# Kernel optimization log

Hardware: AMD Instinct MI355X
Metric: run time of the kernel (lower is better)

Reference implementation:

```python
import jax, jax.numpy as jnp
import numpy as np

HIDDEN = 2048
N_HEADS = 16
N_KV = 4
HEAD_DIM = 128
EPS = 1e-6
B = 8
L = 1024
PREFIX = 256
SUFFIX = L - PREFIX
N_COMPACT = PREFIX + B * SUFFIX  # 6400
T_FULL = B * L                   # 8192
ROPE_THETA = 10000.0


def _radix_indices():
    # full position (b, p) -> compact index
    scatter = np.empty(T_FULL, dtype=np.int64)
    for b in range(B):
        scatter[b * L: b * L + PREFIX] = np.arange(PREFIX)
        scatter[b * L + PREFIX: (b + 1) * L] = PREFIX + b * SUFFIX + np.arange(SUFFIX)
    # compact index -> first full occurrence
    fold = np.empty(N_COMPACT, dtype=np.int64)
    fold[:PREFIX] = np.arange(PREFIX)
    for b in range(B):
        fold[PREFIX + b * SUFFIX: PREFIX + (b + 1) * SUFFIX] = b * L + PREFIX + np.arange(SUFFIX)
    return scatter, fold


def setup_inputs() -> dict:
    key = jax.random.key(0)
    ks = jax.random.split(key, 8)
    scatter_np, fold_np = _radix_indices()
    # per-compact-token positions for RoPE
    pos = np.empty(N_COMPACT, dtype=np.float32)
    pos[:PREFIX] = np.arange(PREFIX)
    for b in range(B):
        pos[PREFIX + b * SUFFIX: PREFIX + (b + 1) * SUFFIX] = PREFIX + np.arange(SUFFIX)
    inv_freq = ROPE_THETA ** (-np.arange(HEAD_DIM // 2, dtype=np.float32) / (HEAD_DIM // 2))
    freqs = pos[:, None] * inv_freq[None, :]  # [N_c, 64]
    s = 0.02
    return {
        "hidden_states": jax.random.normal(ks[0], (N_COMPACT, HIDDEN), jnp.float32),
        "cos": jnp.asarray(np.cos(freqs), jnp.float32),
        "sin": jnp.asarray(np.sin(freqs), jnp.float32),
        "cu_seq_lengths": jnp.arange(B + 1, dtype=jnp.int32) * L,
        "max_seq_len": L,
        "fold_gather": jnp.asarray(fold_np),
        "scatter_indices": jnp.asarray(scatter_np),
        "wq": jax.random.normal(ks[1], (HIDDEN, N_HEADS * HEAD_DIM), jnp.float32) * s,
        "wk": jax.random.normal(ks[2], (HIDDEN, N_KV * HEAD_DIM), jnp.float32) * s,
        "wv": jax.random.normal(ks[3], (HIDDEN, N_KV * HEAD_DIM), jnp.float32) * s,
        "wo": jax.random.normal(ks[4], (N_HEADS * HEAD_DIM, HIDDEN), jnp.float32) * s,
        "q_norm_w": jnp.ones((HEAD_DIM,), jnp.float32),
        "k_norm_w": jnp.ones((HEAD_DIM,), jnp.float32),
    }


def _rmsnorm(x, w):
    xf = x.astype(jnp.float32)
    var = jnp.mean(xf * xf, axis=-1, keepdims=True)
    return (w * (xf * jax.lax.rsqrt(var + EPS))).astype(x.dtype)


def _rope(x, cos, sin):
    # x: [N, H, D]; cos/sin: [N, D/2]
    half = cos.shape[-1]
    x1, x2 = x[..., :half], x[..., half:2 * half]
    c, s = cos[:, None, :], sin[:, None, :]
    return jnp.concatenate([x1 * c - x2 * s, x1 * s + x2 * c], axis=-1)


def reference(hidden_states, cos, sin, cu_seq_lengths, max_seq_len,
              fold_gather, scatter_indices, wq, wk, wv, wo, q_norm_w, k_norm_w):
    N = hidden_states.shape[0]
    q = (hidden_states @ wq).reshape(N, N_HEADS, HEAD_DIM)
    k = (hidden_states @ wk).reshape(N, N_KV, HEAD_DIM)
    v = (hidden_states @ wv).reshape(N, N_KV, HEAD_DIM)
    q = _rope(_rmsnorm(q, q_norm_w), cos, sin)
    k = _rope(_rmsnorm(k, k_norm_w), cos, sin)
    # radix scatter: expand compact tokens to full varlen token stream
    qf = q[scatter_indices].reshape(B, L, N_HEADS, HEAD_DIM)
    kf = k[scatter_indices].reshape(B, L, N_KV, HEAD_DIM)
    vf = v[scatter_indices].reshape(B, L, N_KV, HEAD_DIM)
    group = N_HEADS // N_KV
    kf = jnp.repeat(kf, group, axis=2)
    vf = jnp.repeat(vf, group, axis=2)
    scale = HEAD_DIM ** -0.5
    scores = jnp.einsum('bqhd,bkhd->bhqk', qf, kf) * scale
    causal = jnp.tril(jnp.ones((L, L), dtype=bool))
    scores = jnp.where(causal[None, None], scores, jnp.finfo(scores.dtype).min)
    probs = jax.nn.softmax(scores, axis=-1)
    out = jnp.einsum('bhqk,bkhd->bqhd', probs, vf).reshape(T_FULL, N_HEADS * HEAD_DIM)
    # radix fold: gather back to compact tokens
    out_compact = out[fold_gather]
    return out_compact @ wo
```

## Files before the change

kernel.cpp:

```cpp
#include <hip/hip_runtime.h>
#include <hip/hip_bf16.h>

typedef __bf16 bf16;
typedef __bf16 bf16x4 __attribute__((ext_vector_type(4)));
typedef __bf16 bf16x8 __attribute__((ext_vector_type(8)));
typedef float f32x4 __attribute__((ext_vector_type(4)));

#define HID 2048
#define NHEADS 16
#define NKV 4
#define HD 128
#define NC 6400
#define KVW (NKV * HD)

__device__ __forceinline__ void async_cp16(const bf16* src, bf16* dst_lds) {
  __builtin_amdgcn_global_load_lds(
      (const __attribute__((address_space(1))) void*)src,
      (__attribute__((address_space(3))) void*)dst_lds, 16, 0, 0);
}

__device__ __forceinline__ void xcd_swizzle(int& bx, int& by) {
  int nx = gridDim.x;
  int nwg = nx * gridDim.y;
  int id = by * nx + bx;
  int q = nwg >> 3, r = nwg & 7;
  int xcd = id & 7, idx = id >> 3;
  int nid = (xcd < r ? xcd * (q + 1) : r * (q + 1) + (xcd - r) * q) + idx;
  bx = nid % nx;
  by = nid / nx;
}

__global__ __launch_bounds__(256) void k_cvt(const float* __restrict__ in,
                                             bf16* __restrict__ out) {
  size_t i = ((size_t)blockIdx.x * 256 + threadIdx.x) * 8;
  f32x4 a = *(const f32x4*)(in + i);
  f32x4 b = *(const f32x4*)(in + i + 4);
  bf16x8 t;
  for (int j = 0; j < 4; j++) {
    t[j] = (bf16)a[j];
    t[j + 4] = (bf16)b[j];
  }
  *(bf16x8*)(out + i) = t;
}

__global__ __launch_bounds__(256) void k_transpose(const float* __restrict__ in,
                                                   bf16* __restrict__ out,
                                                   int R, int C) {
  __shared__ bf16 tile[32][33];
  int bc = blockIdx.x * 32, br = blockIdx.y * 32;
  int tx = threadIdx.x & 31, ty = threadIdx.x >> 5;
  for (int i = 0; i < 32; i += 8)
    tile[ty + i][tx] = (bf16)in[(size_t)(br + ty + i) * C + bc + tx];
  __syncthreads();
  for (int i = 0; i < 32; i += 8)
    out[(size_t)(bc + ty + i) * R + br + tx] = tile[tx][ty + i];
}

__device__ __forceinline__ void gemm256_core(
    const bf16* __restrict__ A, const bf16* __restrict__ Bt, int m0, int nloc,
    int K, bf16* AsB, bf16* BsB, f32x4 (&acc)[2][4][4]) {
  const int tid = threadIdx.x;
  const int lane = tid & 63, wave = tid >> 6;
  const int l15 = lane & 15, quad = lane >> 4;
  const int wr = wave >> 2, wc = wave & 3;
  const int r0A = wr * 128 + l15;
  const int r0B = wc * 64 + l15;
  const int colOff0 = (quad * 8) ^ ((l15 & 7) << 3);
  const int colOff1 = (32 + quad * 8) ^ ((l15 & 7) << 3);
  const size_t offS0 =
      (size_t)(tid >> 3) * K + ((((tid & 7) ^ ((tid >> 3) & 7)) << 4) >> 1);
  const size_t offS1 = offS0 + (size_t)64 * K;
  const int dstW0 = wave * 512;
  const int dstW1 = 4096 + wave * 512;
  const bf16* Abase = A + (size_t)m0 * K;
  const bf16* Bbase = Bt + (size_t)nloc * K;
  const int KM = K - 1;

#define STAGE(gb, lds, dbuf, h, kc)                             \
  do {                                                          \
    const bf16* _s = (gb) + (size_t)(h) * 128 * K + (kc);       \
    bf16* _d = (lds) + (dbuf) * 16384 + (h) * 8192;             \
    async_cp16(_s + offS0, _d + dstW0);                         \
    async_cp16(_s + offS1, _d + dstW1);                         \
  } while (0)

#define LDA(dbuf, mh)                                           \
  do {                                                          \
    _Pragma("unroll") for (int i = 0; i < 4; i++) {             \
      int r = r0A + (mh) * 64 + i * 16;                         \
      const bf16* p = AsB + (dbuf) * 16384 + r * 64;            \
      a[i][0] = *(const bf16x8*)(p + colOff0);                  \
      a[i][1] = *(const bf16x8*)(p + colOff1);                  \
    }                                                           \
  } while (0)

#define LDB(dbuf, nh, bb)                                       \
  do {                                                          \
    _Pragma("unroll") for (int j = 0; j < 2; j++) {             \
      int r = r0B + (nh) * 32 + j * 16;                         \
      const bf16* p = BsB + (dbuf) * 16384 + r * 64;            \
      bb[j][0] = *(const bf16x8*)(p + colOff0);                 \
      bb[j][1] = *(const bf16x8*)(p + colOff1);                 \
    }                                                           \
  } while (0)

#define MFMAQ(mh, nh, bb)                                                    \
  do {                                                                       \
    __builtin_amdgcn_s_setprio(1);                                           \
    _Pragma("unroll") for (int i = 0; i < 4; i++)                            \
        _Pragma("unroll") for (int j = 0; j < 2; j++) {                      \
      acc[mh][i][(nh) * 2 + j] = __builtin_amdgcn_mfma_f32_16x16x32_bf16(    \
          a[i][0], bb[j][0], acc[mh][i][(nh) * 2 + j], 0, 0, 0);             \
      acc[mh][i][(nh) * 2 + j] = __builtin_amdgcn_mfma_f32_16x16x32_bf16(    \
          a[i][1], bb[j][1], acc[mh][i][(nh) * 2 + j], 0, 0, 0);             \
    }                                                                        \
    __builtin_amdgcn_s_setprio(0);                                           \
  } while (0)

  STAGE(Abase, AsB, 0, 0, 0);
  STAGE(Abase, AsB, 0, 1, 0);
  STAGE(Bbase, BsB, 0, 0, 0);
  STAGE(Bbase, BsB, 0, 1, 0);
  STAGE(Bbase, BsB, 1, 0, 64);
  STAGE(Bbase, BsB, 1, 1, 64);
  STAGE(Abase, AsB, 1, 0, 64);
  asm volatile("s_waitcnt vmcnt(6)" ::: "memory");
  __builtin_amdgcn_s_barrier();

  bf16x8 a[4][2], b0[2][2], b1[2][2];

  const int NIT = K >> 7;
#pragma unroll 1
  for (int it = 0; it < NIT; ++it) {
    const int kb = it << 7;
    LDA(0, 0);
    LDB(0, 0, b0);
    STAGE(Abase, AsB, 1, 1, (kb + 64) & KM);
    asm volatile("s_waitcnt lgkmcnt(8)");
    __builtin_amdgcn_s_barrier();
    asm volatile("s_waitcnt lgkmcnt(0)" ::: "memory");
    MFMAQ(0, 0, b0);
    __builtin_amdgcn_s_barrier();
    LDB(0, 1, b1);
    __builtin_amdgcn_s_barrier();
    asm volatile("s_waitcnt lgkmcnt(0)" ::: "memory");
    MFMAQ(0, 1, b1);
    __builtin_amdgcn_s_barrier();
    LDA(0, 1);
    STAGE(Bbase, BsB, 0, 0, (kb + 128) & KM);
    __builtin_amdgcn_s_barrier();
    asm volatile("s_waitcnt lgkmcnt(0)" ::: "memory");
    MFMAQ(1, 0, b0);
    __builtin_amdgcn_s_barrier();
    STAGE(Bbase, BsB, 0, 1, (kb + 128) & KM);
    __builtin_amdgcn_s_barrier();
    asm volatile("s_waitcnt lgkmcnt(0)" ::: "memory");
    MFMAQ(1, 1, b1);
    asm volatile("s_waitcnt vmcnt(4)" ::: "memory");
    __builtin_amdgcn_s_barrier();
    LDA(1, 0);
    LDB(1, 0, b0);
    STAGE(Abase, AsB, 0, 0, (kb + 128) & KM);
    asm volatile("s_waitcnt lgkmcnt(8)");
    __builtin_amdgcn_s_barrier();
    asm volatile("s_waitcnt lgkmcnt(0)" ::: "memory");
    MFMAQ(0, 0, b0);
    __builtin_amdgcn_s_barrier();
    LDB(1, 1, b1);
    STAGE(Abase, AsB, 0, 1, (kb + 128) & KM);
    __builtin_amdgcn_s_barrier();
    asm volatile("s_waitcnt lgkmcnt(0)" ::: "memory");
    MFMAQ(0, 1, b1);
    __builtin_amdgcn_s_barrier();
    LDA(1, 1);
    STAGE(Bbase, BsB, 1, 0, (kb + 192) & KM);
    __builtin_amdgcn_s_barrier();
    asm volatile("s_waitcnt lgkmcnt(0)" ::: "memory");
    MFMAQ(1, 0, b0);
    __builtin_amdgcn_s_barrier();
    STAGE(Bbase, BsB, 1, 1, (kb + 192) & KM);
    STAGE(Abase, AsB, 1, 0, (kb + 192) & KM);
    __builtin_amdgcn_s_barrier();
    asm volatile("s_waitcnt lgkmcnt(0)" ::: "memory");
    MFMAQ(1, 1, b1);
    asm volatile("s_waitcnt vmcnt(6)" ::: "memory");
    __builtin_amdgcn_s_barrier();
  }
#undef STAGE
#undef LDA
#undef LDB
#undef MFMAQ
}

__global__ __launch_bounds__(512, 2) void k_proj(const bf16* __restrict__ A,
                                                 const bf16* __restrict__ wqT,
                                                 const bf16* __restrict__ wkT,
                                                 const bf16* __restrict__ wvT,
                                                 bf16* __restrict__ qb,
                                                 bf16* __restrict__ kb,
                                                 bf16* __restrict__ vtb) {
  __shared__ __align__(16) bf16 smem[2][2][256][64];
  int bx = blockIdx.x, by = blockIdx.y;
  xcd_swizzle(bx, by);
  int n0 = bx * 256, m0 = by * 256;

  const bf16* bt;
  int nloc, outsel;
  if (n0 < HID) {
    bt = wqT; nloc = n0; outsel = 0;
  } else if (n0 < HID + KVW) {
    bt = wkT; nloc = n0 - HID; outsel = 1;
  } else {
    bt = wvT; nloc = n0 - HID - KVW; outsel = 2;
  }

  const f32x4 fz = {0.0f, 0.0f, 0.0f, 0.0f};
  f32x4 acc[2][4][4];
#pragma unroll
  for (int mh = 0; mh < 2; mh++)
#pragma unroll
    for (int i = 0; i < 4; i++)
#pragma unroll
      for (int j = 0; j < 4; j++) acc[mh][i][j] = fz;

  gemm256_core(A, bt, m0, nloc, HID, &smem[0][0][0][0], &smem[1][0][0][0], acc);

  int tid = threadIdx.x, lane = tid & 63, wave = tid >> 6;
  int l15 = lane & 15, quad = lane >> 4;
  int wr = wave >> 2, wc = wave & 3;

  if (outsel == 2) {
    asm volatile("s_waitcnt vmcnt(0)" ::: "memory");
    __syncthreads();
    bf16* sm = &smem[0][0][0][0];
#pragma unroll
    for (int mh = 0; mh < 2; mh++)
#pragma unroll
      for (int i = 0; i < 4; i++)
#pragma unroll
        for (int nj = 0; nj < 4; nj++) {
          int col = wc * 64 + nj * 16 + l15;
          int row = wr * 128 + mh * 64 + i * 16 + quad * 4;
          int idx = col * 256 + ((row + ((col & 7) << 3)) & 255);
          bf16x4 v4 = {(bf16)acc[mh][i][nj][0], (bf16)acc[mh][i][nj][1],
                       (bf16)acc[mh][i][nj][2], (bf16)acc[mh][i][nj][3]};
          *(bf16x4*)&sm[idx] = v4;
        }
    __syncthreads();
#pragma unroll
    for (int p = 0; p < 4; p++) {
      int cc = p * 64 + (tid >> 3);
      int h = tid & 7;
#pragma unroll
      for (int j = 0; j < 4; j++) {
        int row8 = h * 32 + j * 8;
        bf16x8 v =
            *(const bf16x8*)&sm[cc * 256 + ((row8 + ((cc & 7) << 3)) & 255)];
        *(bf16x8*)(vtb + (size_t)(nloc + cc) * NC + m0 + row8) = v;
      }
    }
  } else {
#pragma unroll
    for (int mh = 0; mh < 2; mh++)
#pragma unroll
      for (int i = 0; i < 4; i++)
#pragma unroll
        for (int nj = 0; nj < 4; nj++)
#pragma unroll
          for (int r = 0; r < 4; r++) {
            int row = m0 + wr * 128 + mh * 64 + i * 16 + quad * 4 + r;
            int col = nloc + wc * 64 + nj * 16 + l15;
            float v = acc[mh][i][nj][r];
            if (outsel == 0)
              qb[(size_t)row * HID + col] = (bf16)v;
            else
              kb[(size_t)row * KVW + col] = (bf16)v;
          }
  }
}

__global__ __launch_bounds__(512, 2) void k_gemm_out(const bf16* __restrict__ A,
                                                     const bf16* __restrict__ Bt,
                                                     float* __restrict__ C,
                                                     int M, int N, int K) {
  __shared__ __align__(16) bf16 smem[2][2][256][64];
  int bx = blockIdx.x, by = blockIdx.y;
  xcd_swizzle(bx, by);
  int n0 = bx * 256, m0 = by * 256;

  const f32x4 fz = {0.0f, 0.0f, 0.0f, 0.0f};
  f32x4 acc[2][4][4];
#pragma unroll
  for (int mh = 0; mh < 2; mh++)
#pragma unroll
    for (int i = 0; i < 4; i++)
#pragma unroll
      for (int j = 0; j < 4; j++) acc[mh][i][j] = fz;

  gemm256_core(A, Bt, m0, n0, K, &smem[0][0][0][0], &smem[1][0][0][0], acc);

  int tid = threadIdx.x, lane = tid & 63, wave = tid >> 6;
  int l15 = lane & 15, quad = lane >> 4;
  int wr = wave >> 2, wc = wave & 3;
#pragma unroll
  for (int mh = 0; mh < 2; mh++)
#pragma unroll
    for (int i = 0; i < 4; i++)
#pragma unroll
      for (int nj = 0; nj < 4; nj++)
#pragma unroll
        for (int r = 0; r < 4; r++) {
          int row = m0 + wr * 128 + mh * 64 + i * 16 + quad * 4 + r;
          int col = n0 + wc * 64 + nj * 16 + l15;
          C[(size_t)row * N + col] = acc[mh][i][nj][r];
        }
}

__global__ __launch_bounds__(256) void k_normrope(bf16* __restrict__ q,
                                                  bf16* __restrict__ k,
                                                  const float* __restrict__ cs,
                                                  const float* __restrict__ sn,
                                                  const float* __restrict__ qw,
                                                  const float* __restrict__ kw) {
  int pair = blockIdx.x * 4 + (threadIdx.x >> 6);
  int lane = threadIdx.x & 63;
  int n = pair / 20, hh = pair % 20;
  bf16* base;
  const float* w;
  if (hh < 16) {
    base = q + (size_t)n * HID + hh * HD;
    w = qw;
  } else {
    base = k + (size_t)n * KVW + (hh - 16) * HD;
    w = kw;
  }
  float x1 = (float)base[lane], x2 = (float)base[lane + 64];
  float ss = x1 * x1 + x2 * x2;
  for (int o = 32; o; o >>= 1) ss += __shfl_xor(ss, o);
  float inv = rsqrtf(ss * (1.0f / 128.0f) + 1e-6f);
  float x1n = x1 * inv * w[lane];
  float x2n = x2 * inv * w[lane + 64];
  float c = cs[(size_t)n * 64 + lane];
  float s = sn[(size_t)n * 64 + lane];
  base[lane] = (bf16)(x1n * c - x2n * s);
  base[lane + 64] = (bf16)(x1n * s + x2n * c);
}

__global__ __launch_bounds__(256) void k_attn(const bf16* __restrict__ qb,
                                              const bf16* __restrict__ kb,
                                              const bf16* __restrict__ vt,
                                              bf16* __restrict__ ob) {
  int t = blockIdx.x;
  int h = blockIdx.y;
  int kh = h >> 2;
  int tid = threadIdx.x;
  int lane = tid & 63, wave = tid >> 6;
  int l15 = lane & 15, quad = lane >> 4;

  int b, p0, nbase;
  if (t < 96) {
    int ti = 11 - (t >> 3);
    b = t & 7;
    p0 = 256 + ti * 64;
    nbase = 256 + b * 768 + ti * 64;
  } else {
    int pt = 99 - t;
    b = 0;
    p0 = pt * 64;
    nbase = pt * 64;
  }

  __shared__ __align__(16) bf16 Ks[2][64][128];
  __shared__ __align__(16) bf16 Vs[2][128][64];
  __shared__ __align__(16) bf16 Ps[4][16][76];

#define STAGE_KV(buf, kbase)                                                  \
  do {                                                                        \
    _Pragma("unroll") for (int i = 0; i < 4; i++) {                           \
      int rowK = wave * 16 + i * 4 + quad;                                    \
      async_cp16(kb + (size_t)((kbase) + rowK) * KVW + kh * HD +              \
                     ((l15 ^ ((i * 4 + quad) & 7)) << 3),                     \
                 &Ks[buf][0][0] + (wave * 4 + i) * 512);                      \
    }                                                                         \
    _Pragma("unroll") for (int i = 0; i < 4; i++) {                           \
      int dV = wave * 32 + i * 8 + (lane >> 3);                               \
      async_cp16(vt + (size_t)(kh * HD + dV) * NC + (kbase) +                 \
                     (((lane & 7) ^ (lane >> 3)) << 3),                       \
                 &Vs[buf][0][0] + (wave * 4 + i) * 512);                      \
    }                                                                         \
  } while (0)

  const float qscale = 0.08838834764831845f * 1.4426950408889634f;
  bf16x8 aq[4];
  {
    const bf16* qp =
        qb + (size_t)(nbase + wave * 16 + l15) * HID + h * HD + quad * 8;
#pragma unroll
    for (int ks = 0; ks < 4; ks++) {
      bf16x8 v = *(const bf16x8*)(qp + ks * 32);
#pragma unroll
      for (int e = 0; e < 8; e++) v[e] = (bf16)((float)v[e] * qscale);
      aq[ks] = v;
    }
  }
  int qpos[4];
#pragma unroll
  for (int r = 0; r < 4; r++) qpos[r] = p0 + wave * 16 + quad * 4 + r;

  const f32x4 fz = {0.0f, 0.0f, 0.0f, 0.0f};
  f32x4 oacc[8];
#pragma unroll
  for (int i = 0; i < 8; i++) oacc[i] = fz;
  float mrow[4], lrow[4];
#pragma unroll
  for (int r = 0; r < 4; r++) {
    mrow[r] = -3.0e38f;
    lrow[r] = 0.0f;
  }
  const int swzc = (l15 & 7) << 3;

  int nkt = p0 / 64 + 1;

  STAGE_KV(0, 0);
  asm volatile("s_waitcnt vmcnt(0)" ::: "memory");
  __syncthreads();

  int cur = 0;
  for (int kt = 0; kt < nkt; kt++) {
    int kpos0 = kt * 64;
    bool hasnext = (kt + 1 < nkt);
    if (hasnext) {
      int kposN = kpos0 + 64;
      int kbaseN = (kposN < 256) ? kposN : 256 + b * 768 + (kposN - 256);
      STAGE_KV(cur ^ 1, kbaseN);
      __builtin_amdgcn_sched_barrier(0);
    }

    bool diag = (kt == nkt - 1);
    float sv[4][4];
#pragma unroll
    for (int nt = 0; nt < 4; nt++) {
      f32x4 z = fz;
      __builtin_amdgcn_s_setprio(1);
#pragma unroll
      for (int ks = 0; ks < 4; ks++) {
        bf16x8 kf =
            *(const bf16x8*)&Ks[cur][nt * 16 + l15][(ks * 32 + quad * 8) ^ swzc];
        z = __builtin_amdgcn_mfma_f32_16x16x32_bf16(aq[ks], kf, z, 0, 0, 0);
      }
      __builtin_amdgcn_s_setprio(0);
#pragma unroll
      for (int r = 0; r < 4; r++) sv[nt][r] = z[r];
    }
    if (diag) {
#pragma unroll
      for (int nt = 0; nt < 4; nt++) {
        int kpos = kpos0 + nt * 16 + l15;
#pragma unroll
        for (int r = 0; r < 4; r++)
          if (kpos > qpos[r]) sv[nt][r] = -1.0e30f;
      }
    }
    float mx[4];
#pragma unroll
    for (int r = 0; r < 4; r++) {
      float m = fmaxf(fmaxf(sv[0][r], sv[1][r]), fmaxf(sv[2][r], sv[3][r]));
#pragma unroll
      for (int o = 1; o < 16; o <<= 1) m = fmaxf(m, __shfl_xor(m, o));
      mx[r] = m;
    }
    bool ok = (mx[0] <= mrow[0] + 8.0f) && (mx[1] <= mrow[1] + 8.0f) &&
              (mx[2] <= mrow[2] + 8.0f) && (mx[3] <= mrow[3] + 8.0f);
    if (!__all(ok)) {
#pragma unroll
      for (int r = 0; r < 4; r++) {
        float mnew = fmaxf(mrow[r], mx[r]);
        float alpha = exp2f(mrow[r] - mnew);
        mrow[r] = mnew;
        lrow[r] *= alpha;
#pragma unroll
        for (int i = 0; i < 8; i++) oacc[i][r] *= alpha;
      }
    }
#pragma unroll
    for (int r = 0; r < 4; r++) {
      float ps = 0.0f;
#pragma unroll
      for (int nt = 0; nt < 4; nt++) {
        float p = exp2f(sv[nt][r] - mrow[r]);
        sv[nt][r] = p;
        ps += p;
      }
#pragma unroll
      for (int o = 1; o < 16; o <<= 1) ps += __shfl_xor(ps, o);
      lrow[r] += ps;
    }

#pragma unroll
    for (int nt = 0; nt < 4; nt++)
#pragma unroll
      for (int r = 0; r < 4; r++)
        Ps[wave][quad * 4 + r][nt * 16 + l15] = (bf16)sv[nt][r];
    asm volatile("s_waitcnt lgkmcnt(0)" ::: "memory");
    bf16x8 pa[2];
#pragma unroll
    for (int ks = 0; ks < 2; ks++)
      pa[ks] = *(const bf16x8*)&Ps[wave][l15][ks * 32 + quad * 8];
    __builtin_amdgcn_s_setprio(1);
#pragma unroll
    for (int dt = 0; dt < 8; dt++)
#pragma unroll
      for (int ks = 0; ks < 2; ks++) {
        bf16x8 vf =
            *(const bf16x8*)&Vs[cur][dt * 16 + l15][(ks * 32 + quad * 8) ^ swzc];
        oacc[dt] =
            __builtin_amdgcn_mfma_f32_16x16x32_bf16(pa[ks], vf, oacc[dt], 0, 0, 0);
      }
    __builtin_amdgcn_s_setprio(0);

    if (hasnext) {
      asm volatile("s_waitcnt vmcnt(0)" ::: "memory");
      __syncthreads();
      cur ^= 1;
    }
  }
#undef STAGE_KV
#pragma unroll
  for (int r = 0; r < 4; r++) {
    float il = 1.0f / lrow[r];
    bf16* op = ob + (size_t)(nbase + wave * 16 + quad * 4 + r) * HID + h * HD;
#pragma unroll
    for (int dt = 0; dt < 8; dt++) op[dt * 16 + l15] = (bf16)(oacc[dt][r] * il);
  }
}

extern "C" void kernel_launch(void* const* d_in, const int* in_sizes, int n_in,
                              void* d_out, int out_size, void* d_ws,
                              size_t ws_size, hipStream_t stream) {
  const float* hs = (const float*)d_in[0];
  const float* cs = (const float*)d_in[1];
  const float* sn = (const float*)d_in[2];
  const float* wq = (const float*)d_in[7];
  const float* wk = (const float*)d_in[8];
  const float* wv = (const float*)d_in[9];
  const float* wo = (const float*)d_in[10];
  const float* qnw = (const float*)d_in[11];
  const float* knw = (const float*)d_in[12];
  float* out = (float*)d_out;

  bf16* hsb = (bf16*)d_out;
  bf16* wqT = hsb + (size_t)NC * HID;
  bf16* wkT = wqT + (size_t)HID * HID;
  bf16* wvT = wkT + (size_t)KVW * HID;
  bf16* qb  = (bf16*)d_in[0];
  bf16* ab  = qb + (size_t)NC * HID;
  bf16* woT = qb;
  bf16* kb  = (bf16*)d_ws;
  bf16* vtb = kb + (size_t)NC * KVW;

  k_cvt<<<dim3(NC * HID / (256 * 8)), 256, 0, stream>>>(hs, hsb);
  k_transpose<<<dim3(HID / 32, HID / 32), 256, 0, stream>>>(wq, wqT, HID, HID);
  k_transpose<<<dim3(KVW / 32, HID / 32), 256, 0, stream>>>(wk, wkT, HID, KVW);
  k_transpose<<<dim3(KVW / 32, HID / 32), 256, 0, stream>>>(wv, wvT, HID, KVW);

  k_proj<<<dim3((HID + 2 * KVW) / 256, NC / 256), 512, 0, stream>>>(
      hsb, wqT, wkT, wvT, qb, kb, vtb);

  k_normrope<<<dim3(NC * 20 / 4), 256, 0, stream>>>(qb, kb, cs, sn, qnw, knw);

  k_attn<<<dim3(100, NHEADS), 256, 0, stream>>>(qb, kb, vtb, ab);

  k_transpose<<<dim3(HID / 32, HID / 32), 256, 0, stream>>>(wo, woT, HID, HID);

  k_gemm_out<<<dim3(HID / 256, NC / 256), 512, 0, stream>>>(ab, woT, out, NC, HID, HID);
}
```

Measured before the change: 457.8 us.

## Process 128 query rows per attention block to reuse staged K/V tiles

The attention kernel now gives each wave two 16-row query groups, so a block covers 128 query rows and the grid halves. Each K/V tile staged in LDS is reused for twice as many queries, which cuts global K/V traffic and staging overhead. The change also uses raw v_exp_f32 for the softmax exponentials and sets launch bounds to two blocks per CU. In exchange, register pressure roughly doubles for the accumulators, the grid has fewer blocks for load balancing, and the last two key tiles need causal masking instead of one.

```diff
diff --git a/kernel.cpp b/kernel.cpp
--- a/kernel.cpp
+++ b/kernel.cpp
@@ -17,6 +17,12 @@
   __builtin_amdgcn_global_load_lds(
       (const __attribute__((address_space(1))) void*)src,
       (__attribute__((address_space(3))) void*)dst_lds, 16, 0, 0);
+}
+
+__device__ __forceinline__ float exp2_hw(float x) {
+  float r;
+  asm("v_exp_f32 %0, %1" : "=v"(r) : "v"(x));
+  return r;
 }
 
 __device__ __forceinline__ void xcd_swizzle(int& bx, int& by) {
@@ -346,10 +352,10 @@
   base[lane + 64] = (bf16)(x1n * s + x2n * c);
 }
 
-__global__ __launch_bounds__(256) void k_attn(const bf16* __restrict__ qb,
-                                              const bf16* __restrict__ kb,
-                                              const bf16* __restrict__ vt,
-                                              bf16* __restrict__ ob) {
+__global__ __launch_bounds__(256, 2) void k_attn(const bf16* __restrict__ qb,
+                                                 const bf16* __restrict__ kb,
+                                                 const bf16* __restrict__ vt,
+                                                 bf16* __restrict__ ob) {
   int t = blockIdx.x;
   int h = blockIdx.y;
   int kh = h >> 2;
@@ -358,16 +364,16 @@
   int l15 = lane & 15, quad = lane >> 4;
 
   int b, p0, nbase;
-  if (t < 96) {
-    int ti = 11 - (t >> 3);
+  if (t < 48) {
+    int ti = 5 - (t >> 3);
     b = t & 7;
-    p0 = 256 + ti * 64;
-    nbase = 256 + b * 768 + ti * 64;
+    p0 = 256 + ti * 128;
+    nbase = 256 + b * 768 + ti * 128;
   } else {
-    int pt = 99 - t;
+    int pt = 49 - t;
     b = 0;
-    p0 = pt * 64;
-    nbase = pt * 64;
+    p0 = pt * 128;
+    nbase = pt * 128;
   }
 
   __shared__ __align__(16) bf16 Ks[2][64][128];
@@ -391,35 +397,43 @@
   } while (0)
 
   const float qscale = 0.08838834764831845f * 1.4426950408889634f;
-  bf16x8 aq[4];
-  {
-    const bf16* qp =
-        qb + (size_t)(nbase + wave * 16 + l15) * HID + h * HD + quad * 8;
+  bf16x8 aq[2][4];
+#pragma unroll
+  for (int rg = 0; rg < 2; rg++) {
+    const bf16* qp = qb +
+        (size_t)(nbase + wave * 32 + rg * 16 + l15) * HID + h * HD + quad * 8;
 #pragma unroll
     for (int ks = 0; ks < 4; ks++) {
       bf16x8 v = *(const bf16x8*)(qp + ks * 32);
 #pragma unroll
       for (int e = 0; e < 8; e++) v[e] = (bf16)((float)v[e] * qscale);
-      aq[ks] = v;
-    }
-  }
-  int qpos[4];
-#pragma unroll
-  for (int r = 0; r < 4; r++) qpos[r] = p0 + wave * 16 + quad * 4 + r;
+      aq[rg][ks] = v;
+    }
+  }
+  int qpos[2][4];
+#pragma unroll
+  for (int rg = 0; rg < 2; rg++)
+#pragma unroll
+    for (int r = 0; r < 4; r++)
+      qpos[rg][r] = p0 + wave * 32 + rg * 16 + quad * 4 + r;
 
   const f32x4 fz = {0.0f, 0.0f, 0.0f, 0.0f};
-  f32x4 oacc[8];
-#pragma unroll
-  for (int i = 0; i < 8; i++) oacc[i] = fz;
-  float mrow[4], lrow[4];
-#pragma unroll
-  for (int r = 0; r < 4; r++) {
-    mrow[r] = -3.0e38f;
-    lrow[r] = 0.0f;
-  }
+  f32x4 oacc[2][8];
+#pragma unroll
+  for (int rg = 0; rg < 2; rg++)
+#pragma unroll
+    for (int i = 0; i < 8; i++) oacc[rg][i] = fz;
+  float mrow[2][4], lrow[2][4];
+#pragma unroll
+  for (int rg = 0; rg < 2; rg++)
+#pragma unroll
+    for (int r = 0; r < 4; r++) {
+      mrow[rg][r] = -3.0e38f;
+      lrow[rg][r] = 0.0f;
+    }
   const int swzc = (l15 & 7) << 3;
 
-  int nkt = p0 / 64 + 1;
+  int nkt = p0 / 64 + 2;
 
   STAGE_KV(0, 0);
   asm volatile("s_waitcnt vmcnt(0)" ::: "memory");
@@ -436,87 +450,90 @@
       __builtin_amdgcn_sched_barrier(0);
     }
 
-    bool diag = (kt == nkt - 1);
-    float sv[4][4];
-#pragma unroll
-    for (int nt = 0; nt < 4; nt++) {
-      f32x4 z = fz;
+    bool masked = (kpos0 >= p0);
+#pragma unroll
+    for (int rg = 0; rg < 2; rg++) {
+      float sv[4][4];
+#pragma unroll
+      for (int nt = 0; nt < 4; nt++) {
+        f32x4 z = fz;
+        __builtin_amdgcn_s_setprio(1);
+#pragma unroll
+        for (int ks = 0; ks < 4; ks++) {
+          bf16x8 kf = *(const bf16x8*)&Ks[cur][nt * 16 + l15]
+                                        [(ks * 32 + quad * 8) ^ swzc];
+          z = __builtin_amdgcn_mfma_f32_16x16x32_bf16(aq[rg][ks], kf, z, 0, 0, 0);
+        }
+        __builtin_amdgcn_s_setprio(0);
+#pragma unroll
+        for (int r = 0; r < 4; r++) sv[nt][r] = z[r];
+      }
+      if (masked) {
+#pragma unroll
+        for (int nt = 0; nt < 4; nt++) {
+          int kpos = kpos0 + nt * 16 + l15;
+#pragma unroll
+          for (int r = 0; r < 4; r++)
+            if (kpos > qpos[rg][r]) sv[nt][r] = -1.0e30f;
+        }
+      }
+      float mx[4];
+#pragma unroll
+      for (int r = 0; r < 4; r++) {
+        float m = fmaxf(fmaxf(sv[0][r], sv[1][r]), fmaxf(sv[2][r], sv[3][r]));
+#pragma unroll
+        for (int o = 1; o < 16; o <<= 1) m = fmaxf(m, __shfl_xor(m, o));
+        mx[r] = m;
+      }
+      bool ok = (mx[0] <= mrow[rg][0] + 8.0f) && (mx[1] <= mrow[rg][1] + 8.0f) &&
+                (mx[2] <= mrow[rg][2] + 8.0f) && (mx[3] <= mrow[rg][3] + 8.0f);
+      if (!__all(ok)) {
+#pragma unroll
+        for (int r = 0; r < 4; r++) {
+          float mnew = fmaxf(mrow[rg][r], mx[r]);
+          float alpha = exp2_hw(mrow[rg][r] - mnew);
+          mrow[rg][r] = mnew;
+          lrow[rg][r] *= alpha;
+#pragma unroll
+          for (int i = 0; i < 8; i++) oacc[rg][i][r] *= alpha;
+        }
+      }
+#pragma unroll
+      for (int r = 0; r < 4; r++) {
+        float ps = 0.0f;
+#pragma unroll
+        for (int nt = 0; nt < 4; nt++) {
+          float p = exp2_hw(sv[nt][r] - mrow[rg][r]);
+          sv[nt][r] = p;
+          ps += p;
+        }
+#pragma unroll
+        for (int o = 1; o < 16; o <<= 1) ps += __shfl_xor(ps, o);
+        lrow[rg][r] += ps;
+      }
+
+#pragma unroll
+      for (int nt = 0; nt < 4; nt++)
+#pragma unroll
+        for (int r = 0; r < 4; r++)
+          Ps[wave][quad * 4 + r][nt * 16 + l15] = (bf16)sv[nt][r];
+      asm volatile("s_waitcnt lgkmcnt(0)" ::: "memory");
+      bf16x8 pa[2];
+#pragma unroll
+      for (int ks = 0; ks < 2; ks++)
+        pa[ks] = *(const bf16x8*)&Ps[wave][l15][ks * 32 + quad * 8];
       __builtin_amdgcn_s_setprio(1);
 #pragma unroll
-      for (int ks = 0; ks < 4; ks++) {
-        bf16x8 kf =
-            *(const bf16x8*)&Ks[cur][nt * 16 + l15][(ks * 32 + quad * 8) ^ swzc];
-        z = __builtin_amdgcn_mfma_f32_16x16x32_bf16(aq[ks], kf, z, 0, 0, 0);
-      }
+      for (int dt = 0; dt < 8; dt++)
+#pragma unroll
+        for (int ks = 0; ks < 2; ks++) {
+          bf16x8 vf = *(const bf16x8*)&Vs[cur][dt * 16 + l15]
+                                        [(ks * 32 + quad * 8) ^ swzc];
+          oacc[rg][dt] = __builtin_amdgcn_mfma_f32_16x16x32_bf16(
+              pa[ks], vf, oacc[rg][dt], 0, 0, 0);
+        }
       __builtin_amdgcn_s_setprio(0);
-#pragma unroll
-      for (int r = 0; r < 4; r++) sv[nt][r] = z[r];
-    }
-    if (diag) {
-#pragma unroll
-      for (int nt = 0; nt < 4; nt++) {
-        int kpos = kpos0 + nt * 16 + l15;
-#pragma unroll
-        for (int r = 0; r < 4; r++)
-          if (kpos > qpos[r]) sv[nt][r] = -1.0e30f;
-      }
-    }
-    float mx[4];
-#pragma unroll
-    for (int r = 0; r < 4; r++) {
-      float m = fmaxf(fmaxf(sv[0][r], sv[1][r]), fmaxf(sv[2][r], sv[3][r]));
-#pragma unroll
-      for (int o = 1; o < 16; o <<= 1) m = fmaxf(m, __shfl_xor(m, o));
-      mx[r] = m;
-    }
-    bool ok = (mx[0] <= mrow[0] + 8.0f) && (mx[1] <= mrow[1] + 8.0f) &&
-              (mx[2] <= mrow[2] + 8.0f) && (mx[3] <= mrow[3] + 8.0f);
-    if (!__all(ok)) {
-#pragma unroll
-      for (int r = 0; r < 4; r++) {
-        float mnew = fmaxf(mrow[r], mx[r]);
-        float alpha = exp2f(mrow[r] - mnew);
-        mrow[r] = mnew;
-        lrow[r] *= alpha;
-#pragma unroll
-        for (int i = 0; i < 8; i++) oacc[i][r] *= alpha;
-      }
-    }
-#pragma unroll
-    for (int r = 0; r < 4; r++) {
-      float ps = 0.0f;
-#pragma unroll
-      for (int nt = 0; nt < 4; nt++) {
-        float p = exp2f(sv[nt][r] - mrow[r]);
-        sv[nt][r] = p;
-        ps += p;
-      }
-#pragma unroll
-      for (int o = 1; o < 16; o <<= 1) ps += __shfl_xor(ps, o);
-      lrow[r] += ps;
-    }
-
-#pragma unroll
-    for (int nt = 0; nt < 4; nt++)
-#pragma unroll
-      for (int r = 0; r < 4; r++)
-        Ps[wave][quad * 4 + r][nt * 16 + l15] = (bf16)sv[nt][r];
-    asm volatile("s_waitcnt lgkmcnt(0)" ::: "memory");
-    bf16x8 pa[2];
-#pragma unroll
-    for (int ks = 0; ks < 2; ks++)
-      pa[ks] = *(const bf16x8*)&Ps[wave][l15][ks * 32 + quad * 8];
-    __builtin_amdgcn_s_setprio(1);
-#pragma unroll
-    for (int dt = 0; dt < 8; dt++)
-#pragma unroll
-      for (int ks = 0; ks < 2; ks++) {
-        bf16x8 vf =
-            *(const bf16x8*)&Vs[cur][dt * 16 + l15][(ks * 32 + quad * 8) ^ swzc];
-        oacc[dt] =
-            __builtin_amdgcn_mfma_f32_16x16x32_bf16(pa[ks], vf, oacc[dt], 0, 0, 0);
-      }
-    __builtin_amdgcn_s_setprio(0);
+    }
 
     if (hasnext) {
       asm volatile("s_waitcnt vmcnt(0)" ::: "memory");
@@ -526,12 +543,16 @@
   }
 #undef STAGE_KV
 #pragma unroll
-  for (int r = 0; r < 4; r++) {
-    float il = 1.0f / lrow[r];
-    bf16* op = ob + (size_t)(nbase + wave * 16 + quad * 4 + r) * HID + h * HD;
-#pragma unroll
-    for (int dt = 0; dt < 8; dt++) op[dt * 16 + l15] = (bf16)(oacc[dt][r] * il);
-  }
+  for (int rg = 0; rg < 2; rg++)
+#pragma unroll
+    for (int r = 0; r < 4; r++) {
+      float il = 1.0f / lrow[rg][r];
+      bf16* op = ob +
+          (size_t)(nbase + wave * 32 + rg * 16 + quad * 4 + r) * HID + h * HD;
+#pragma unroll
+      for (int dt = 0; dt < 8; dt++)
+        op[dt * 16 + l15] = (bf16)(oacc[rg][dt][r] * il);
+    }
 }
 
 extern "C" void kernel_launch(void* const* d_in, const int* in_sizes, int n_in,
@@ -568,7 +589,7 @@
 
   k_normrope<<<dim3(NC * 20 / 4), 256, 0, stream>>>(qb, kb, cs, sn, qnw, knw);
 
-  k_attn<<<dim3(100, NHEADS), 256, 0, stream>>>(qb, kb, vtb, ab);
+  k_attn<<<dim3(50, NHEADS), 256, 0, stream>>>(qb, kb, vtb, ab);
 
   k_transpose<<<dim3(HID / 32, HID / 32), 256, 0, stream>>>(wo, woT, HID, HID);
 
```

After: 457.7 us. About the same (-0.0%).
